# Kernel tuning notes

Hardware: AMD Instinct MI355X
Metric: run time of the kernel (lower is better)

## Reference

```python
import jax, jax.numpy as jnp
import numpy as np

NUM_TAGS = 64
SEQ_LEN = 512
BATCH = 512


def setup_inputs() -> dict:
    key = jax.random.key(0)
    k1, k2, k3, k4, k5 = jax.random.split(key, 5)
    emissions = jax.random.normal(k1, (SEQ_LEN, BATCH, NUM_TAGS), dtype=jnp.float32)
    tags = jax.random.randint(k2, (SEQ_LEN, BATCH), 0, NUM_TAGS, dtype=jnp.int32)
    mask = jnp.ones((SEQ_LEN, BATCH), dtype=jnp.int32)
    start_transitions = jax.random.uniform(k3, (NUM_TAGS,), dtype=jnp.float32)
    end_transitions = jax.random.uniform(k4, (NUM_TAGS,), dtype=jnp.float32)
    transitions = jax.random.uniform(k5, (NUM_TAGS, NUM_TAGS), dtype=jnp.float32)
    return {
        "emissions": emissions,
        "tags": tags,
        "mask": mask,
        "start_transitions": start_transitions,
        "end_transitions": end_transitions,
        "transitions": transitions,
    }


def _compute_score(emissions, tags, mask, start_transitions, end_transitions, transitions):
    # emissions: (S,B,T), tags/mask: (S,B)
    seq_length, batch_size = tags.shape
    maskf = mask.astype(jnp.float32)
    barange = jnp.arange(batch_size)
    # emission scores for gold tags at every step: (S,B)
    emit = jnp.take_along_axis(emissions, tags[:, :, None], axis=2)[:, :, 0]
    # transition scores between consecutive gold tags: (S-1,B)
    trans = transitions[tags[:-1], tags[1:]]
    score = start_transitions[tags[0]] + emit[0]
    score = score + ((trans + emit[1:]) * maskf[1:]).sum(axis=0)
    seq_ends = mask.astype(jnp.int32).sum(axis=0) - 1  # (B,)
    last_tags = tags[seq_ends, barange]
    score = score + end_transitions[last_tags]
    return score  # (B,)


def _compute_normalizer(emissions, mask, start_transitions, end_transitions, transitions):
    # sequential forward-algorithm scan over time
    score0 = start_transitions + emissions[0]  # (B,T)

    def step(score, inp):
        em, m = inp  # em: (B,T), m: (B,)
        # (B,Tprev,Tnext) logsumexp over Tprev
        next_score = jax.nn.logsumexp(
            score[:, :, None] + transitions[None, :, :] + em[:, None, :], axis=1
        )
        score = jnp.where(m[:, None].astype(bool), next_score, score)
        return score, None

    score, _ = jax.lax.scan(step, score0, (emissions[1:], mask[1:]))
    return jax.nn.logsumexp(score + end_transitions, axis=1)  # (B,)


def reference(emissions, tags, mask, start_transitions, end_transitions, transitions):
    numerator = _compute_score(emissions, tags, mask, start_transitions, end_transitions, transitions)
    denominator = _compute_normalizer(emissions, mask, start_transitions, end_transitions, transitions)
    llh = numerator - denominator
    return llh.sum()  # reduction='sum'
```

## Files before the change

kernel.cpp:

```cpp
#include <hip/hip_runtime.h>

#define T   512
#define B   512
#define NT  64
#define QS  16
#define NQ  (T / QS)
#define RING 4

typedef _Float16 h2 __attribute__((ext_vector_type(2)));

__device__ __forceinline__ float rflf(float x) {
    return __uint_as_float(__builtin_amdgcn_readfirstlane(__float_as_uint(x)));
}

__device__ __forceinline__ float dot2(h2 a, h2 b, float c) {
#if __has_builtin(__builtin_amdgcn_fdot2)
    return __builtin_amdgcn_fdot2(a, b, c, false);
#else
    return c + (float)a.x * (float)b.x + (float)a.y * (float)b.y;
#endif
}

__global__ __launch_bounds__(64) void crf_fused(
    const float* __restrict__ emissions,
    const int*   __restrict__ tags,
    const int*   __restrict__ mask,
    const float* __restrict__ startT,
    const float* __restrict__ endT,
    const float* __restrict__ trans,
    float* __restrict__ out)
{
    const int j = threadIdx.x;

    __shared__ __align__(16) float ebuf[RING][QS][NT];

    if (blockIdx.x < B) {
        const int b = blockIdx.x;

        h2 Eh[NT / 2];
#pragma unroll
        for (int m = 0; m < NT / 2; ++m) {
            Eh[m].x = (_Float16)__expf(trans[(2 * m)     * NT + j]);
            Eh[m].y = (_Float16)__expf(trans[(2 * m + 1) * NT + j]);
        }

        const int jr = j >> 4;
        const int c0 = (j & 15) * 4;
        float4 sA[4];

        auto issue_q = [&](int g) {
#pragma unroll
            for (int k = 0; k < 4; ++k) {
                const int t = g * QS + 4 * k + jr;
                sA[k] = *(const float4*)&emissions[((size_t)t * B + b) * NT + c0];
            }
        };
        auto write_q = [&](int g) {
#pragma unroll
            for (int k = 0; k < 4; ++k) {
                float4 w;
                w.x = __expf(sA[k].x); w.y = __expf(sA[k].y);
                w.z = __expf(sA[k].z); w.w = __expf(sA[k].w);
                *(float4*)&ebuf[g & (RING - 1)][4 * k + jr][c0] = w;
            }
        };

        for (int g = 0; g < 3; ++g) { issue_q(g); write_q(g); }
        issue_q(3);

        const float e0  = emissions[(size_t)b * NT + j];
        const float sc0 = startT[j] + e0;
        const float S0  = rflf(sc0);
        float q = __expf(sc0 - S0);
        int   K = 0;

        int pk_i;
        {
            const int qi = __float_as_int(q);
            const int qo = __builtin_amdgcn_update_dpp(0, qi, 0xB1, 0xF, 0xF, true);
            pk_i = __builtin_bit_cast(int,
                    __builtin_amdgcn_cvt_pkrtz(q, __int_as_float(qo)));
        }

        int mpre = mask[j * B + b];
        unsigned long long mbc = 0;

        for (int x = 0; x < NQ; ++x) {
            const int gw = (x + 3 < NQ) ? x + 3 : NQ - 1;
            write_q(gw);
            const int gl = (x + 4 < NQ) ? x + 4 : NQ - 1;
            issue_q(gl);

            if ((x & 3) == 0) {
                mbc = __ballot(mpre != 0);
                const int cn = ((x >> 2) + 1 < 8) ? (x >> 2) + 1 : 7;
                mpre = mask[(cn * 64 + j) * B + b];
            }

            const int tt0 = (x == 0) ? 1 : 0;
#pragma unroll 4
            for (int tt = tt0; tt < QS; ++tt) {
                const float X = ebuf[x & (RING - 1)][tt][j];

                float a0 = 0.f, a1 = 0.f, a2 = 0.f, a3 = 0.f;
#pragma unroll
                for (int n = 0; n < 8; ++n) {
                    const int u0 = __builtin_amdgcn_readlane(pk_i, 8 * n + 0);
                    const int u1 = __builtin_amdgcn_readlane(pk_i, 8 * n + 2);
                    const int u2 = __builtin_amdgcn_readlane(pk_i, 8 * n + 4);
                    const int u3 = __builtin_amdgcn_readlane(pk_i, 8 * n + 6);
                    a0 = dot2(__builtin_bit_cast(h2, u0), Eh[4 * n + 0], a0);
                    a1 = dot2(__builtin_bit_cast(h2, u1), Eh[4 * n + 1], a1);
                    a2 = dot2(__builtin_bit_cast(h2, u2), Eh[4 * n + 2], a2);
                    a3 = dot2(__builtin_bit_cast(h2, u3), Eh[4 * n + 3], a3);
                }
                const float p = (a0 + a1) + (a2 + a3);

                const int bits = __builtin_amdgcn_readfirstlane(__float_as_int(p));
                const int k    = ((bits >> 23) & 255) - 127;
                const float r  = __int_as_float((127 - k) << 23);

                const int  ttc = ((x & 3) << 4) + tt;
                const bool mc  = (mbc >> ttc) & 1ull;
                const float qn = p * r * X;
                q = mc ? qn : q;
                K += mc ? k : 0;

                const int qi = __float_as_int(q);
                const int qo = __builtin_amdgcn_update_dpp(0, qi, 0xB1, 0xF, 0xF, true);
                pk_i = __builtin_bit_cast(int,
                        __builtin_amdgcn_cvt_pkrtz(q, __int_as_float(qo)));
            }
        }

        float v = q * __expf(endT[j]);
#pragma unroll
        for (int off = 32; off > 0; off >>= 1)
            v += __shfl_xor(v, off);
        if (j == 0)
            atomicAdd(out, -(S0 + (float)K * 0.69314718f + __logf(v)));

    } else {
        const int b = blockIdx.x - B;

        float acc = 0.f;
        int   cnt = 0;
#pragma unroll
        for (int m = 0; m < T / 64; ++m) {
            const int t  = j + 64 * m;
            const int mv = mask[t * B + b];
            const int tg = tags[t * B + b];
            cnt += (int)__popcll(__ballot(mv != 0));
            if (t == 0) {
                acc += startT[tg] + emissions[(size_t)b * NT + tg];
            } else if (mv) {
                const int tp = tags[(t - 1) * B + b];
                acc += trans[tp * NT + tg]
                     + emissions[(size_t)(t * B + b) * NT + tg];
            }
        }
#pragma unroll
        for (int off = 32; off > 0; off >>= 1)
            acc += __shfl_xor(acc, off);
        if (j == 0) {
            const int last = tags[(size_t)(cnt - 1) * B + b];
            atomicAdd(out, acc + endT[last]);
        }
    }
}

extern "C" void kernel_launch(void* const* d_in, const int* in_sizes, int n_in,
                              void* d_out, int out_size, void* d_ws, size_t ws_size,
                              hipStream_t stream) {
    const float* emissions = (const float*)d_in[0];
    const int*   tags      = (const int*)  d_in[1];
    const int*   mask      = (const int*)  d_in[2];
    const float* startT    = (const float*)d_in[3];
    const float* endT      = (const float*)d_in[4];
    const float* trans     = (const float*)d_in[5];
    float* out = (float*)d_out;

    hipMemsetAsync(out, 0, sizeof(float), stream);
    crf_fused<<<2 * B, 64, 0, stream>>>(
        emissions, tags, mask, startT, endT, trans, out);
}
```

Baseline: 194.6 us.

## Compute forward-algorithm matvec with bf16 MFMA and renormalize every four steps

Replaces the per-step 64x64 mat-vec, which used readlane broadcasts and fp16 dot2 instructions, with eight bf16 16x16x32 MFMA ops. The probability vector is gathered into MFMA A-fragments with ds_bpermute, and the exp(transitions) B-fragments are kept in registers. Exponent renormalization via readfirstlane now runs every four steps instead of every step, taking a scalar dependency off most iterations. In exchange, bf16 packing truncates q (lower precision than the old fp16), and the step now depends on LDS-permute and MFMA latency.

```diff
diff --git a/kernel.cpp b/kernel.cpp
--- a/kernel.cpp
+++ b/kernel.cpp
@@ -7,18 +7,20 @@
 #define NQ  (T / QS)
 #define RING 4
 
-typedef _Float16 h2 __attribute__((ext_vector_type(2)));
+typedef short bf16x8 __attribute__((ext_vector_type(8)));
+typedef float f32x4  __attribute__((ext_vector_type(4)));
 
 __device__ __forceinline__ float rflf(float x) {
     return __uint_as_float(__builtin_amdgcn_readfirstlane(__float_as_uint(x)));
 }
 
-__device__ __forceinline__ float dot2(h2 a, h2 b, float c) {
-#if __has_builtin(__builtin_amdgcn_fdot2)
-    return __builtin_amdgcn_fdot2(a, b, c, false);
-#else
-    return c + (float)a.x * (float)b.x + (float)a.y * (float)b.y;
-#endif
+__device__ __forceinline__ unsigned rne_bf16(float f) {
+    unsigned u = __float_as_uint(f);
+    u += 0x7fffu + ((u >> 16) & 1u);
+    return u >> 16;
+}
+__device__ __forceinline__ int pk_bf16_rne(float lo, float hi) {
+    return (int)(rne_bf16(lo) | (rne_bf16(hi) << 16));
 }
 
 __global__ __launch_bounds__(64) void crf_fused(
@@ -35,24 +37,36 @@
     __shared__ __align__(16) float ebuf[RING][QS][NT];
 
     if (blockIdx.x < B) {
-        const int b = blockIdx.x;
-
-        h2 Eh[NT / 2];
-#pragma unroll
-        for (int m = 0; m < NT / 2; ++m) {
-            Eh[m].x = (_Float16)__expf(trans[(2 * m)     * NT + j]);
-            Eh[m].y = (_Float16)__expf(trans[(2 * m + 1) * NT + j]);
-        }
-
-        const int jr = j >> 4;
-        const int c0 = (j & 15) * 4;
+        const int b    = blockIdx.x;
+        const int n    = j & 15;
+        const int quad = j >> 4;
+
+        bf16x8 Bf[4][2];
+#pragma unroll
+        for (int nt = 0; nt < 4; ++nt)
+#pragma unroll
+            for (int h = 0; h < 2; ++h) {
+                int dw[4];
+#pragma unroll
+                for (int e2 = 0; e2 < 4; ++e2) {
+                    const int k0 = h * 32 + quad * 8 + 2 * e2;
+                    const float v0 = __expf(trans[k0 * NT + nt * 16 + n]);
+                    const float v1 = __expf(trans[(k0 + 1) * NT + nt * 16 + n]);
+                    dw[e2] = pk_bf16_rne(v0, v1);
+                }
+                int4 t4 = {dw[0], dw[1], dw[2], dw[3]};
+                Bf[nt][h] = __builtin_bit_cast(bf16x8, t4);
+            }
+
+        const int jr   = j >> 4;
+        const int col0 = (j & 15) * 4;
         float4 sA[4];
 
         auto issue_q = [&](int g) {
 #pragma unroll
             for (int k = 0; k < 4; ++k) {
                 const int t = g * QS + 4 * k + jr;
-                sA[k] = *(const float4*)&emissions[((size_t)t * B + b) * NT + c0];
+                sA[k] = *(const float4*)&emissions[((size_t)t * B + b) * NT + col0];
             }
         };
         auto write_q = [&](int g) {
@@ -61,7 +75,7 @@
                 float4 w;
                 w.x = __expf(sA[k].x); w.y = __expf(sA[k].y);
                 w.z = __expf(sA[k].z); w.w = __expf(sA[k].w);
-                *(float4*)&ebuf[g & (RING - 1)][4 * k + jr][c0] = w;
+                *(float4*)&ebuf[g & (RING - 1)][4 * k + jr][col0] = w;
             }
         };
 
@@ -74,13 +88,7 @@
         float q = __expf(sc0 - S0);
         int   K = 0;
 
-        int pk_i;
-        {
-            const int qi = __float_as_int(q);
-            const int qo = __builtin_amdgcn_update_dpp(0, qi, 0xB1, 0xF, 0xF, true);
-            pk_i = __builtin_bit_cast(int,
-                    __builtin_amdgcn_cvt_pkrtz(q, __int_as_float(qo)));
-        }
+        const int base0 = quad * 8 * 4;
 
         int mpre = mask[j * B + b];
         unsigned long long mbc = 0;
@@ -102,34 +110,47 @@
             for (int tt = tt0; tt < QS; ++tt) {
                 const float X = ebuf[x & (RING - 1)][tt][j];
 
-                float a0 = 0.f, a1 = 0.f, a2 = 0.f, a3 = 0.f;
-#pragma unroll
-                for (int n = 0; n < 8; ++n) {
-                    const int u0 = __builtin_amdgcn_readlane(pk_i, 8 * n + 0);
-                    const int u1 = __builtin_amdgcn_readlane(pk_i, 8 * n + 2);
-                    const int u2 = __builtin_amdgcn_readlane(pk_i, 8 * n + 4);
-                    const int u3 = __builtin_amdgcn_readlane(pk_i, 8 * n + 6);
-                    a0 = dot2(__builtin_bit_cast(h2, u0), Eh[4 * n + 0], a0);
-                    a1 = dot2(__builtin_bit_cast(h2, u1), Eh[4 * n + 1], a1);
-                    a2 = dot2(__builtin_bit_cast(h2, u2), Eh[4 * n + 2], a2);
-                    a3 = dot2(__builtin_bit_cast(h2, u3), Eh[4 * n + 3], a3);
+                const int qi    = __float_as_int(q);
+                const int qswap = __builtin_amdgcn_update_dpp(0, qi, 0xB1, 0xF, 0xF, true);
+                const int pk    = __builtin_amdgcn_perm(
+                                     (unsigned)qswap, (unsigned)qi, 0x07060302u);
+                int f0[4], f1[4];
+#pragma unroll
+                for (int d = 0; d < 4; ++d) {
+                    f0[d] = __builtin_amdgcn_ds_bpermute(base0 + 8 * d, pk);
+                    f1[d] = __builtin_amdgcn_ds_bpermute(base0 + 8 * d + 128, pk);
                 }
-                const float p = (a0 + a1) + (a2 + a3);
-
-                const int bits = __builtin_amdgcn_readfirstlane(__float_as_int(p));
-                const int k    = ((bits >> 23) & 255) - 127;
-                const float r  = __int_as_float((127 - k) << 23);
+                int4 i40 = {f0[0], f0[1], f0[2], f0[3]};
+                int4 i41 = {f1[0], f1[1], f1[2], f1[3]};
+                const bf16x8 a0 = __builtin_bit_cast(bf16x8, i40);
+                const bf16x8 a1 = __builtin_bit_cast(bf16x8, i41);
+
+                const f32x4 z = {0.f, 0.f, 0.f, 0.f};
+                f32x4 c0 = __builtin_amdgcn_mfma_f32_16x16x32_bf16(a0, Bf[0][0], z, 0, 0, 0);
+                f32x4 c1 = __builtin_amdgcn_mfma_f32_16x16x32_bf16(a0, Bf[1][0], z, 0, 0, 0);
+                f32x4 c2 = __builtin_amdgcn_mfma_f32_16x16x32_bf16(a0, Bf[2][0], z, 0, 0, 0);
+                f32x4 c3 = __builtin_amdgcn_mfma_f32_16x16x32_bf16(a0, Bf[3][0], z, 0, 0, 0);
+                c0 = __builtin_amdgcn_mfma_f32_16x16x32_bf16(a1, Bf[0][1], c0, 0, 0, 0);
+                c1 = __builtin_amdgcn_mfma_f32_16x16x32_bf16(a1, Bf[1][1], c1, 0, 0, 0);
+                c2 = __builtin_amdgcn_mfma_f32_16x16x32_bf16(a1, Bf[2][1], c2, 0, 0, 0);
+                c3 = __builtin_amdgcn_mfma_f32_16x16x32_bf16(a1, Bf[3][1], c3, 0, 0, 0);
+
+                float p = c0[0];
+                p = (quad == 1) ? c1[0] : p;
+                p = (quad == 2) ? c2[0] : p;
+                p = (quad == 3) ? c3[0] : p;
 
                 const int  ttc = ((x & 3) << 4) + tt;
                 const bool mc  = (mbc >> ttc) & 1ull;
-                const float qn = p * r * X;
+                const float qn = p * X;
                 q = mc ? qn : q;
-                K += mc ? k : 0;
-
-                const int qi = __float_as_int(q);
-                const int qo = __builtin_amdgcn_update_dpp(0, qi, 0xB1, 0xF, 0xF, true);
-                pk_i = __builtin_bit_cast(int,
-                        __builtin_amdgcn_cvt_pkrtz(q, __int_as_float(qo)));
+
+                if ((tt & 3) == 3) {
+                    const int bits = __builtin_amdgcn_readfirstlane(__float_as_int(q));
+                    const int k    = ((bits >> 23) & 255) - 127;
+                    q *= __int_as_float((127 - k) << 23);
+                    K += k;
+                }
             }
         }
 
```

After: 195.1 us. About the same (+0.3%).
